# Kernel tuning notes

Hardware: AMD Instinct MI355X
Metric: run time of the kernel (lower is better)

The kernel has to match this reference:

```python
import jax, jax.numpy as jnp
import numpy as np

B, S, D = 16, 4096, 1024
K = 65536  # number of keys == number of concepts (identity mapping)
EPS = 1e-12


def setup_inputs() -> dict:
    key = jax.random.key(0)
    k1, k2, k3, k4, k5, k6 = jax.random.split(key, 6)
    return {
        "hidden": jax.random.normal(k1, (B, S, D), dtype=jnp.float32),
        "concept_signal": jax.random.normal(k2, (B, 1, D), dtype=jnp.float32),
        "keys": jax.random.normal(k3, (K, D), dtype=jnp.float32),
        "values": jax.random.normal(k4, (K, 1, D), dtype=jnp.float32),
        "key_to_value": jnp.arange(K, dtype=jnp.int64),
        "W_layer": jax.random.normal(k5, (D, D), dtype=jnp.float32) * 0.02,
        "b_layer": jax.random.normal(k6, (D,), dtype=jnp.float32) * 0.02,
    }


def _l2norm(x, axis=-1):
    return x / jnp.maximum(jnp.linalg.norm(x, axis=axis, keepdims=True), EPS)


def reference(hidden, concept_signal, keys, values, key_to_value, W_layer, b_layer):
    # self.layer(hidden_state): Linear(D, D)
    layer_out = jnp.einsum("bsd,ed->bse", hidden, W_layer) + b_layer  # [B, S, D]

    # Tensor branch of forward: per-sample nearest-key search.
    # q: one query position per sample (P=1) -> [B, D]
    q = concept_signal[:, 0, :]
    cos = jnp.einsum("bd,kd->bk", _l2norm(q), _l2norm(keys))  # cosine similarity [B, K]
    dist = 1.0 - cos                                           # cosine distance
    chosen_key = jnp.argmin(dist, axis=1)                      # [B] nearest key per sample
    # s = 1 - smallest_dist; with threshold=-2.0 it always passes; with
    # max_tokens_per_concept=1, k = max(1, ceil(clamp(s,0,1)*1)) == 1 token.
    concept_idx = key_to_value[chosen_key]                     # [B]
    tokens = values[concept_idx, 0, :]                         # [B, D] (first of the k=1 tokens)
    tokens = _l2norm(tokens)                                   # F.normalize(..., p=2, dim=-1)
    # vstack one token onto each sample, then stack -> [B, S+1, D]
    return jnp.concatenate([layer_out, tokens[:, None, :]], axis=1)
```

## Files before the change

kernel.cpp:

```cpp
#include <hip/hip_runtime.h>

constexpr int BB = 16;
constexpr int SS = 4096;
constexpr int DD = 1024;
constexpr int KK = 65536;
constexpr int GM = BB * SS;
constexpr int GK = DD;

typedef __attribute__((ext_vector_type(8))) short bf16x8;
typedef __attribute__((ext_vector_type(4))) float f32x4;
typedef __attribute__((ext_vector_type(8))) unsigned short ushort8;

#define GLD_LDS16(g, l)                                                        \
  __builtin_amdgcn_global_load_lds(                                            \
      (const __attribute__((address_space(1))) void*)(g),                      \
      (__attribute__((address_space(3))) void*)(l), 16, 0, 0)

__device__ __forceinline__ unsigned short f2bf(float x) {
  unsigned u = __float_as_uint(x);
  u += 0x7fffu + ((u >> 16) & 1u);
  return (unsigned short)(u >> 16);
}

__global__ void cvt_bf16(const float* __restrict__ in,
                         unsigned short* __restrict__ out, int n8) {
  int stride = gridDim.x * blockDim.x;
  for (int i = blockIdx.x * blockDim.x + threadIdx.x; i < n8; i += stride) {
    const float4* p = (const float4*)in + (size_t)i * 2;
    float4 a = p[0], b = p[1];
    ushort8 r;
    r[0] = f2bf(a.x); r[1] = f2bf(a.y); r[2] = f2bf(a.z); r[3] = f2bf(a.w);
    r[4] = f2bf(b.x); r[5] = f2bf(b.y); r[6] = f2bf(b.z); r[7] = f2bf(b.w);
    *(ushort8*)(out + (size_t)i * 8) = r;
  }
}

__global__ __launch_bounds__(256) void qt_prep(const float* __restrict__ csig,
                                               float* __restrict__ qT) {
  int e = blockIdx.x * 256 + threadIdx.x;
  int b = e >> 10, d = e & 1023;
  qT[d * 16 + b] = csig[e];
}

__global__ __launch_bounds__(256) void gemm_bt(
    const unsigned short* __restrict__ A,
    const unsigned short* __restrict__ Bm,
    const float* __restrict__ bias,
    float* __restrict__ out) {
  __shared__ unsigned short sA[128 * 32];
  __shared__ unsigned short sB[128 * 32];

  int g = blockIdx.x;
  int t = ((g & 7) << 9) + (g >> 3);
  int mt = t >> 3, nt = t & 7;
  int m0 = mt << 7, n0 = nt << 7;

  int tid = threadIdx.x, lane = tid & 63, wv = tid >> 6;
  int wr = wv >> 1, wc = wv & 1;
  int fr = lane & 15, ko = (lane >> 4) << 3;

  f32x4 acc[4][4] = {};

  int srow[2], scol[2];
  for (int i = 0; i < 2; ++i) {
    int off = (wv << 11) + (i << 10) + (lane << 4);
    srow[i] = off >> 6;
    scol[i] = (off & 63) >> 1;
  }

  for (int kt = 0; kt < GK / 32; ++kt) {
    int k0 = kt << 5;
    for (int i = 0; i < 2; ++i) {
      unsigned short* ldsA = sA + (wv << 10) + (i << 9);
      unsigned short* ldsB = sB + (wv << 10) + (i << 9);
      GLD_LDS16(A + (size_t)(m0 + srow[i]) * GK + k0 + scol[i], ldsA);
      GLD_LDS16(Bm + (size_t)(n0 + srow[i]) * GK + k0 + scol[i], ldsB);
    }
    __syncthreads();

    bf16x8 af[4], bfr[4];
#pragma unroll
    for (int i = 0; i < 4; ++i) {
      af[i]  = *(const bf16x8*)&sA[((wr << 6) + (i << 4) + fr) * 32 + ko];
      bfr[i] = *(const bf16x8*)&sB[((wc << 6) + (i << 4) + fr) * 32 + ko];
    }
#pragma unroll
    for (int m = 0; m < 4; ++m)
#pragma unroll
      for (int n = 0; n < 4; ++n)
        acc[m][n] = __builtin_amdgcn_mfma_f32_16x16x32_bf16(af[m], bfr[n],
                                                            acc[m][n], 0, 0, 0);
    __syncthreads();
  }

  int r0 = (lane >> 4) << 2, c = lane & 15;
#pragma unroll
  for (int n = 0; n < 4; ++n) {
    int gcol = n0 + (wc << 6) + (n << 4) + c;
    float bv = bias[gcol];
#pragma unroll
    for (int m = 0; m < 4; ++m) {
      int gr = m0 + (wr << 6) + (m << 4) + r0;
#pragma unroll
      for (int j = 0; j < 4; ++j) {
        int grow = gr + j;
        size_t o = ((size_t)(grow + (grow >> 12)) << 10) + gcol;
        out[o] = acc[m][n][j] + bv;
      }
    }
  }
}

__global__ __launch_bounds__(256) void cos_scores(
    const float* __restrict__ keys,
    const float* __restrict__ qT,
    float* __restrict__ pscore,
    int* __restrict__ pidx) {
  constexpr int DT = 32;
  __shared__ float kt[DT][256];
  __shared__ float rs[4][16];
  __shared__ int   ri[4][16];

  int tid = threadIdx.x, lane = tid & 63, w = tid >> 6;
  int k0 = blockIdx.x * 256;

  float acc[16] = {0.f, 0.f, 0.f, 0.f, 0.f, 0.f, 0.f, 0.f,
                   0.f, 0.f, 0.f, 0.f, 0.f, 0.f, 0.f, 0.f};
  float nrm = 0.f;

  int srow = tid >> 3, scol = (tid & 7) << 2;
  const float* gsrc = keys + (size_t)(k0 + srow) * DD + scol;

  float4 stg[8];
#pragma unroll
  for (int i = 0; i < 8; ++i)
    stg[i] = *(const float4*)(gsrc + (size_t)i * 32 * DD);

  for (int t = 0; t < DD / DT; ++t) {
#pragma unroll
    for (int i = 0; i < 8; ++i) {
      int r = (i << 5) + srow;
#pragma unroll
      for (int j = 0; j < 4; ++j) {
        int dd = scol + j;
        kt[dd][r ^ (((dd >> 2) & 7) << 2)] = stg[i][j];
      }
    }
    __syncthreads();

    if (t + 1 < DD / DT) {
      int d0n = (t + 1) * DT;
#pragma unroll
      for (int i = 0; i < 8; ++i)
        stg[i] = *(const float4*)(gsrc + (size_t)i * 32 * DD + d0n);
    }

    const float* qrow = qT + t * DT * 16;
#pragma unroll
    for (int dd = 0; dd < DT; ++dd) {
      float kv = kt[dd][tid ^ (((dd >> 2) & 7) << 2)];
      float4 q0 = *(const float4*)(qrow + dd * 16 + 0);
      float4 q1 = *(const float4*)(qrow + dd * 16 + 4);
      float4 q2 = *(const float4*)(qrow + dd * 16 + 8);
      float4 q3 = *(const float4*)(qrow + dd * 16 + 12);
      acc[0] = fmaf(kv, q0.x, acc[0]);   acc[1] = fmaf(kv, q0.y, acc[1]);
      acc[2] = fmaf(kv, q0.z, acc[2]);   acc[3] = fmaf(kv, q0.w, acc[3]);
      acc[4] = fmaf(kv, q1.x, acc[4]);   acc[5] = fmaf(kv, q1.y, acc[5]);
      acc[6] = fmaf(kv, q1.z, acc[6]);   acc[7] = fmaf(kv, q1.w, acc[7]);
      acc[8] = fmaf(kv, q2.x, acc[8]);   acc[9] = fmaf(kv, q2.y, acc[9]);
      acc[10] = fmaf(kv, q2.z, acc[10]); acc[11] = fmaf(kv, q2.w, acc[11]);
      acc[12] = fmaf(kv, q3.x, acc[12]); acc[13] = fmaf(kv, q3.y, acc[13]);
      acc[14] = fmaf(kv, q3.z, acc[14]); acc[15] = fmaf(kv, q3.w, acc[15]);
      nrm = fmaf(kv, kv, nrm);
    }
    __syncthreads();
  }

  float inv = rsqrtf(fmaxf(nrm, 1e-24f));
#pragma unroll
  for (int b = 0; b < 16; ++b) {
    float s = acc[b] * inv;
    int i = k0 + tid;
#pragma unroll
    for (int off = 32; off; off >>= 1) {
      float s2 = __shfl_xor(s, off);
      int i2 = __shfl_xor(i, off);
      if (s2 > s || (s2 == s && i2 < i)) { s = s2; i = i2; }
    }
    if (lane == 0) { rs[w][b] = s; ri[w][b] = i; }
  }
  __syncthreads();
  if (tid < 16) {
    float bs = rs[0][tid]; int bi = ri[0][tid];
#pragma unroll
    for (int w2 = 1; w2 < 4; ++w2) {
      float s = rs[w2][tid]; int i = ri[w2][tid];
      if (s > bs || (s == bs && i < bi)) { bs = s; bi = i; }
    }
    pscore[(size_t)tid * gridDim.x + blockIdx.x] = bs;
    pidx[(size_t)tid * gridDim.x + blockIdx.x] = bi;
  }
}

__global__ __launch_bounds__(256) void select_write(
    const float* __restrict__ pscore, const int* __restrict__ pidx, int nb,
    const int* __restrict__ ktv, const float* __restrict__ values,
    float* __restrict__ out) {
  __shared__ float ss[4];
  __shared__ int si[4];
  __shared__ float snrm;
  __shared__ int swin;
  int b = blockIdx.x, tid = threadIdx.x, lane = tid & 63, wv = tid >> 6;

  float best = -1e30f;
  int bidx = 0x7fffffff;
  for (int t = tid; t < nb; t += 256) {
    float s = pscore[(size_t)b * nb + t];
    int i = pidx[(size_t)b * nb + t];
    if (s > best || (s == best && i < bidx)) { best = s; bidx = i; }
  }
#pragma unroll
  for (int off = 32; off; off >>= 1) {
    float s = __shfl_xor(best, off);
    int i = __shfl_xor(bidx, off);
    if (s > best || (s == best && i < bidx)) { best = s; bidx = i; }
  }
  if (lane == 0) { ss[wv] = best; si[wv] = bidx; }
  __syncthreads();
  if (tid == 0) {
    float bs = ss[0]; int bi = si[0];
    for (int w2 = 1; w2 < 4; ++w2)
      if (ss[w2] > bs || (ss[w2] == bs && si[w2] < bi)) { bs = ss[w2]; bi = si[w2]; }
    swin = ktv[bi];
  }
  __syncthreads();
  int idx = swin;

  float4 v = ((const float4*)(values + (size_t)idx * DD))[tid];
  float nrm = v.x * v.x + v.y * v.y + v.z * v.z + v.w * v.w;
#pragma unroll
  for (int off = 32; off; off >>= 1) nrm += __shfl_xor(nrm, off);
  if (lane == 0) ss[wv] = nrm;
  __syncthreads();
  if (tid == 0) snrm = rsqrtf(fmaxf(ss[0] + ss[1] + ss[2] + ss[3], 1e-24f));
  __syncthreads();
  float inv = snrm;

  float4 o;
  o.x = v.x * inv; o.y = v.y * inv; o.z = v.z * inv; o.w = v.w * inv;
  ((float4*)(out + (((size_t)b * (SS + 1) + SS) << 10)))[tid] = o;
}

extern "C" void kernel_launch(void* const* d_in, const int* in_sizes, int n_in,
                              void* d_out, int out_size, void* d_ws,
                              size_t ws_size, hipStream_t stream) {
  const float* hidden = (const float*)d_in[0];
  const float* csig   = (const float*)d_in[1];
  const float* keys   = (const float*)d_in[2];
  const float* values = (const float*)d_in[3];
  const int*   ktv    = (const int*)d_in[4];
  const float* W      = (const float*)d_in[5];
  const float* bias   = (const float*)d_in[6];
  float* out = (float*)d_out;

  char* ws = (char*)d_ws;
  unsigned short* hbf = (unsigned short*)ws;
  unsigned short* wbf = (unsigned short*)(ws + (size_t)GM * GK * 2);
  char* p = ws + (size_t)GM * GK * 2 + (size_t)DD * GK * 2;
  float* pscore = (float*)p;
  int* pidx = (int*)(p + 16 * 256 * sizeof(float));
  float* qT = (float*)(p + 2 * 16 * 256 * sizeof(float));

  cvt_bf16<<<4096, 256, 0, stream>>>(hidden, hbf, GM * GK / 8);
  cvt_bf16<<<512, 256, 0, stream>>>(W, wbf, DD * GK / 8);
  qt_prep<<<64, 256, 0, stream>>>(csig, qT);

  cos_scores<<<256, 256, 0, stream>>>(keys, qT, pscore, pidx);

  gemm_bt<<<(GM / 128) * (DD / 128), 256, 0, stream>>>(hbf, wbf, bias, out);

  select_write<<<BB, 256, 0, stream>>>(pscore, pidx, 256, ktv, values, out);
}
```

Before: 464.9 us.

## Replace GEMM with 256x256 pipelined 8-wave kernel and split cosine search over D

The bf16 GEMM moves from a 128x128 tile with 4 waves and full-barrier k-steps to a 256x256 tile with 8 waves. It uses a 64-wide k, double-buffered swizzled LDS staging, interleaved async global-to-LDS loads, and setprio/sched_barrier phase scheduling, aiming to raise MFMA utilisation and operand reuse. Separately, the cosine key scan is split into four D-chunks across 1024 blocks with q staged in LDS, followed by a combine kernel that does the argmax. This is meant to fill more CUs than the old 256-block launch, at the cost of extra partial-sum traffic and one more launch.

```diff
diff --git a/kernel.cpp b/kernel.cpp
--- a/kernel.cpp
+++ b/kernel.cpp
@@ -42,101 +42,186 @@
   qT[d * 16 + b] = csig[e];
 }
 
-__global__ __launch_bounds__(256) void gemm_bt(
+
+#define LDA8(AH, BUF) do {                                                     \
+  _Pragma("unroll") for (int ms = 0; ms < 4; ++ms) {                           \
+    int rowa = (wm << 7) + ((AH) << 6) + (ms << 4) + fr;                       \
+    _Pragma("unroll") for (int ks = 0; ks < 2; ++ks) {                         \
+      int ia = ((rowa << 6) + (ks << 5) + (kg << 3)) ^ sw;                     \
+      ar[ms * 2 + ks] = *(const bf16x8*)&lds[(BUF) + ia]; } }                  \
+} while (0)
+
+#define LDB4(NP, BUF) do {                                                     \
+  _Pragma("unroll") for (int nn = 0; nn < 2; ++nn) {                           \
+    int rowb = (wn << 6) + ((((NP) << 1) + nn) << 4) + fr;                     \
+    _Pragma("unroll") for (int ks = 0; ks < 2; ++ks) {                         \
+      int ib = ((rowb << 6) + (ks << 5) + (kg << 3)) ^ sw;                     \
+      br[(((NP) << 1) + nn) * 2 + ks] = *(const bf16x8*)&lds[(BUF) + ib]; } }  \
+} while (0)
+
+#define MFMAQ(AH, NP) do {                                                     \
+  _Pragma("unroll") for (int ms = 0; ms < 4; ++ms)                             \
+  _Pragma("unroll") for (int nn = 0; nn < 2; ++nn)                             \
+  _Pragma("unroll") for (int ks = 0; ks < 2; ++ks)                             \
+    acc[((AH) << 2) + ms][((NP) << 1) + nn] =                                  \
+      __builtin_amdgcn_mfma_f32_16x16x32_bf16(ar[ms * 2 + ks],                 \
+        br[(((NP) << 1) + nn) * 2 + ks],                                       \
+        acc[((AH) << 2) + ms][((NP) << 1) + nn], 0, 0, 0);                     \
+} while (0)
+
+#define STAGEQ(GB, LB, QJ)                                                     \
+  GLD_LDS16((GB) + (size_t)(((QJ) << 6) + srq) * GK + ssc,                     \
+            &lds[(LB) + ((((QJ) << 9) + (wv << 6)) << 3)])
+
+#define PH_MID do { __builtin_amdgcn_s_barrier();                              \
+  asm volatile("s_waitcnt lgkmcnt(0)" ::: "memory");                           \
+  __builtin_amdgcn_sched_barrier(0);                                           \
+  __builtin_amdgcn_s_setprio(1); } while (0)
+
+#define PH_END do { __builtin_amdgcn_s_setprio(0);                             \
+  __builtin_amdgcn_s_barrier(); } while (0)
+
+#define PH_END_V(N) do { __builtin_amdgcn_s_setprio(0);                        \
+  asm volatile("s_waitcnt vmcnt(" #N ")" ::: "memory");                        \
+  __builtin_amdgcn_sched_barrier(0);                                           \
+  __builtin_amdgcn_s_barrier(); } while (0)
+
+__global__ __launch_bounds__(512, 2) void gemm8(
     const unsigned short* __restrict__ A,
     const unsigned short* __restrict__ Bm,
     const float* __restrict__ bias,
     float* __restrict__ out) {
-  __shared__ unsigned short sA[128 * 32];
-  __shared__ unsigned short sB[128 * 32];
+  __shared__ unsigned short lds[65536];
 
   int g = blockIdx.x;
-  int t = ((g & 7) << 9) + (g >> 3);
-  int mt = t >> 3, nt = t & 7;
-  int m0 = mt << 7, n0 = nt << 7;
+  int t = ((g & 7) << 7) + (g >> 3);
+  int mt = t >> 2, nt = t & 3;
+  int m0 = mt << 8, n0 = nt << 8;
 
   int tid = threadIdx.x, lane = tid & 63, wv = tid >> 6;
-  int wr = wv >> 1, wc = wv & 1;
-  int fr = lane & 15, ko = (lane >> 4) << 3;
-
-  f32x4 acc[4][4] = {};
-
-  int srow[2], scol[2];
-  for (int i = 0; i < 2; ++i) {
-    int off = (wv << 11) + (i << 10) + (lane << 4);
-    srow[i] = off >> 6;
-    scol[i] = (off & 63) >> 1;
-  }
-
-  for (int kt = 0; kt < GK / 32; ++kt) {
-    int k0 = kt << 5;
-    for (int i = 0; i < 2; ++i) {
-      unsigned short* ldsA = sA + (wv << 10) + (i << 9);
-      unsigned short* ldsB = sB + (wv << 10) + (i << 9);
-      GLD_LDS16(A + (size_t)(m0 + srow[i]) * GK + k0 + scol[i], ldsA);
-      GLD_LDS16(Bm + (size_t)(n0 + srow[i]) * GK + k0 + scol[i], ldsB);
-    }
-    __syncthreads();
-
-    bf16x8 af[4], bfr[4];
-#pragma unroll
-    for (int i = 0; i < 4; ++i) {
-      af[i]  = *(const bf16x8*)&sA[((wr << 6) + (i << 4) + fr) * 32 + ko];
-      bfr[i] = *(const bf16x8*)&sB[((wc << 6) + (i << 4) + fr) * 32 + ko];
-    }
-#pragma unroll
-    for (int m = 0; m < 4; ++m)
-#pragma unroll
-      for (int n = 0; n < 4; ++n)
-        acc[m][n] = __builtin_amdgcn_mfma_f32_16x16x32_bf16(af[m], bfr[n],
-                                                            acc[m][n], 0, 0, 0);
-    __syncthreads();
-  }
-
-  int r0 = (lane >> 4) << 2, c = lane & 15;
-#pragma unroll
-  for (int n = 0; n < 4; ++n) {
-    int gcol = n0 + (wc << 6) + (n << 4) + c;
+  int wm = wv >> 2, wn = wv & 3;
+  int fr = lane & 15, kg = lane >> 4;
+  int sw = (fr & 7) << 3;
+
+  int srq = (wv << 3) + (lane >> 3);
+  int ssc = (((lane & 7) ^ ((lane >> 3) & 7)) << 3);
+
+  const unsigned short* Ag = A + (size_t)m0 * GK;
+  const unsigned short* Bg = Bm + (size_t)n0 * GK;
+
+  f32x4 acc[8][4] = {};
+  bf16x8 ar[8], br[8];
+
+  {
+    const unsigned short* b0 = Bg;
+    const unsigned short* a1 = Ag + 64;
+    const unsigned short* b1 = Bg + 64;
+    STAGEQ(Ag, 0, 0); STAGEQ(Ag, 0, 1); STAGEQ(Ag, 0, 2); STAGEQ(Ag, 0, 3);
+    STAGEQ(b0, 16384, 0); STAGEQ(b0, 16384, 1);
+    STAGEQ(b0, 16384, 2); STAGEQ(b0, 16384, 3);
+    STAGEQ(a1, 32768, 0); STAGEQ(a1, 32768, 2);
+    STAGEQ(b1, 49152, 0); STAGEQ(b1, 49152, 1);
+    STAGEQ(b1, 49152, 2); STAGEQ(b1, 49152, 3);
+    asm volatile("s_waitcnt vmcnt(6)" ::: "memory");
+    __builtin_amdgcn_sched_barrier(0);
+    __builtin_amdgcn_s_barrier();
+  }
+
+  for (int i = 0; i < 7; ++i) {
+    const unsigned short* a1 = Ag + (size_t)(2 * i + 1) * 64;
+    const unsigned short* a2 = Ag + (size_t)(2 * i + 2) * 64;
+    const unsigned short* b2 = Bg + (size_t)(2 * i + 2) * 64;
+    const unsigned short* a3 = Ag + (size_t)(2 * i + 3) * 64;
+    const unsigned short* b3 = Bg + (size_t)(2 * i + 3) * 64;
+    LDA8(0, 0); LDB4(0, 16384);
+    STAGEQ(a1, 32768, 1); STAGEQ(a1, 32768, 3);
+    PH_MID; MFMAQ(0, 0); PH_END;
+    LDB4(1, 16384);
+    STAGEQ(a2, 0, 0); STAGEQ(a2, 0, 2);
+    PH_MID; MFMAQ(0, 1); PH_END;
+    LDA8(1, 0);
+    STAGEQ(b2, 16384, 0); STAGEQ(b2, 16384, 1);
+    PH_MID; MFMAQ(1, 0); PH_END;
+    STAGEQ(b2, 16384, 2); STAGEQ(b2, 16384, 3);
+    PH_MID; MFMAQ(1, 1); PH_END_V(6);
+    LDA8(0, 32768); LDB4(0, 49152);
+    STAGEQ(a2, 0, 1); STAGEQ(a2, 0, 3);
+    PH_MID; MFMAQ(0, 0); PH_END;
+    LDB4(1, 49152);
+    STAGEQ(a3, 32768, 0); STAGEQ(a3, 32768, 2);
+    PH_MID; MFMAQ(0, 1); PH_END;
+    LDA8(1, 32768);
+    STAGEQ(b3, 49152, 0); STAGEQ(b3, 49152, 1);
+    PH_MID; MFMAQ(1, 0); PH_END;
+    STAGEQ(b3, 49152, 2); STAGEQ(b3, 49152, 3);
+    PH_MID; MFMAQ(1, 1); PH_END_V(6);
+  }
+
+  {
+    const unsigned short* a15 = Ag + (size_t)15 * 64;
+    LDA8(0, 0); LDB4(0, 16384);
+    STAGEQ(a15, 32768, 1); STAGEQ(a15, 32768, 3);
+    PH_MID; MFMAQ(0, 0); PH_END;
+    LDB4(1, 16384); PH_MID; MFMAQ(0, 1); PH_END;
+    LDA8(1, 0);     PH_MID; MFMAQ(1, 0); PH_END;
+    PH_MID; MFMAQ(1, 1); PH_END_V(0);
+    LDA8(0, 32768); LDB4(0, 49152); PH_MID; MFMAQ(0, 0); PH_END;
+    LDB4(1, 49152); PH_MID; MFMAQ(0, 1); PH_END;
+    LDA8(1, 32768); PH_MID; MFMAQ(1, 0); PH_END;
+    PH_MID; MFMAQ(1, 1);
+    __builtin_amdgcn_s_setprio(0);
+  }
+
+  int r0 = kg << 2, cc = fr;
+#pragma unroll
+  for (int ni = 0; ni < 4; ++ni) {
+    int gcol = n0 + (wn << 6) + (ni << 4) + cc;
     float bv = bias[gcol];
 #pragma unroll
-    for (int m = 0; m < 4; ++m) {
-      int gr = m0 + (wr << 6) + (m << 4) + r0;
+    for (int mi = 0; mi < 8; ++mi) {
+      int gr = m0 + (wm << 7) + (mi << 4) + r0;
 #pragma unroll
       for (int j = 0; j < 4; ++j) {
         int grow = gr + j;
         size_t o = ((size_t)(grow + (grow >> 12)) << 10) + gcol;
-        out[o] = acc[m][n][j] + bv;
+        out[o] = acc[mi][ni][j] + bv;
       }
     }
   }
 }
 
-__global__ __launch_bounds__(256) void cos_scores(
+__global__ __launch_bounds__(256) void cos_part4(
     const float* __restrict__ keys,
     const float* __restrict__ qT,
-    float* __restrict__ pscore,
-    int* __restrict__ pidx) {
-  constexpr int DT = 32;
-  __shared__ float kt[DT][256];
-  __shared__ float rs[4][16];
-  __shared__ int   ri[4][16];
-
-  int tid = threadIdx.x, lane = tid & 63, w = tid >> 6;
-  int k0 = blockIdx.x * 256;
+    float* __restrict__ pd,
+    float* __restrict__ pn) {
+  __shared__ float kt[32][256];
+  __shared__ float qs[256 * 16];
+
+  int tid = threadIdx.x;
+  int kgrp = blockIdx.x & 255, dc = blockIdx.x >> 8;
+  int k0 = kgrp << 8, d0 = dc << 8;
+
+  {
+    const float4* src = (const float4*)(qT + (size_t)d0 * 16);
+    float4* dst = (float4*)qs;
+#pragma unroll
+    for (int i = 0; i < 4; ++i) dst[tid + i * 256] = src[tid + i * 256];
+  }
 
   float acc[16] = {0.f, 0.f, 0.f, 0.f, 0.f, 0.f, 0.f, 0.f,
                    0.f, 0.f, 0.f, 0.f, 0.f, 0.f, 0.f, 0.f};
   float nrm = 0.f;
 
   int srow = tid >> 3, scol = (tid & 7) << 2;
-  const float* gsrc = keys + (size_t)(k0 + srow) * DD + scol;
+  const float* gsrc = keys + (size_t)(k0 + srow) * DD + d0 + scol;
 
   float4 stg[8];
 #pragma unroll
   for (int i = 0; i < 8; ++i)
     stg[i] = *(const float4*)(gsrc + (size_t)i * 32 * DD);
 
-  for (int t = 0; t < DD / DT; ++t) {
+  for (int t = 0; t < 8; ++t) {
 #pragma unroll
     for (int i = 0; i < 8; ++i) {
       int r = (i << 5) + srow;
@@ -148,26 +233,25 @@
     }
     __syncthreads();
 
-    if (t + 1 < DD / DT) {
-      int d0n = (t + 1) * DT;
+    if (t + 1 < 8) {
 #pragma unroll
       for (int i = 0; i < 8; ++i)
-        stg[i] = *(const float4*)(gsrc + (size_t)i * 32 * DD + d0n);
-    }
-
-    const float* qrow = qT + t * DT * 16;
-#pragma unroll
-    for (int dd = 0; dd < DT; ++dd) {
+        stg[i] = *(const float4*)(gsrc + (size_t)i * 32 * DD + (t + 1) * 32);
+    }
+
+    const float* qb = qs + (t << 5) * 16;
+#pragma unroll
+    for (int dd = 0; dd < 32; ++dd) {
       float kv = kt[dd][tid ^ (((dd >> 2) & 7) << 2)];
-      float4 q0 = *(const float4*)(qrow + dd * 16 + 0);
-      float4 q1 = *(const float4*)(qrow + dd * 16 + 4);
-      float4 q2 = *(const float4*)(qrow + dd * 16 + 8);
-      float4 q3 = *(const float4*)(qrow + dd * 16 + 12);
-      acc[0] = fmaf(kv, q0.x, acc[0]);   acc[1] = fmaf(kv, q0.y, acc[1]);
-      acc[2] = fmaf(kv, q0.z, acc[2]);   acc[3] = fmaf(kv, q0.w, acc[3]);
-      acc[4] = fmaf(kv, q1.x, acc[4]);   acc[5] = fmaf(kv, q1.y, acc[5]);
-      acc[6] = fmaf(kv, q1.z, acc[6]);   acc[7] = fmaf(kv, q1.w, acc[7]);
-      acc[8] = fmaf(kv, q2.x, acc[8]);   acc[9] = fmaf(kv, q2.y, acc[9]);
+      float4 q0 = *(const float4*)(qb + dd * 16 + 0);
+      float4 q1 = *(const float4*)(qb + dd * 16 + 4);
+      float4 q2 = *(const float4*)(qb + dd * 16 + 8);
+      float4 q3 = *(const float4*)(qb + dd * 16 + 12);
+      acc[0]  = fmaf(kv, q0.x, acc[0]);  acc[1]  = fmaf(kv, q0.y, acc[1]);
+      acc[2]  = fmaf(kv, q0.z, acc[2]);  acc[3]  = fmaf(kv, q0.w, acc[3]);
+      acc[4]  = fmaf(kv, q1.x, acc[4]);  acc[5]  = fmaf(kv, q1.y, acc[5]);
+      acc[6]  = fmaf(kv, q1.z, acc[6]);  acc[7]  = fmaf(kv, q1.w, acc[7]);
+      acc[8]  = fmaf(kv, q2.x, acc[8]);  acc[9]  = fmaf(kv, q2.y, acc[9]);
       acc[10] = fmaf(kv, q2.z, acc[10]); acc[11] = fmaf(kv, q2.w, acc[11]);
       acc[12] = fmaf(kv, q3.x, acc[12]); acc[13] = fmaf(kv, q3.y, acc[13]);
       acc[14] = fmaf(kv, q3.z, acc[14]); acc[15] = fmaf(kv, q3.w, acc[15]);
@@ -176,11 +260,43 @@
     __syncthreads();
   }
 
+  int k = k0 + tid;
+  float4* po = (float4*)(pd + ((size_t)dc * KK + k) * 16);
+  po[0] = make_float4(acc[0], acc[1], acc[2], acc[3]);
+  po[1] = make_float4(acc[4], acc[5], acc[6], acc[7]);
+  po[2] = make_float4(acc[8], acc[9], acc[10], acc[11]);
+  po[3] = make_float4(acc[12], acc[13], acc[14], acc[15]);
+  pn[(size_t)dc * KK + k] = nrm;
+}
+
+__global__ __launch_bounds__(256) void cos_combine(
+    const float* __restrict__ pd, const float* __restrict__ pn,
+    float* __restrict__ pscore, int* __restrict__ pidx) {
+  __shared__ float rs[4][16];
+  __shared__ int ri[4][16];
+  int tid = threadIdx.x, lane = tid & 63, w = tid >> 6;
+  int k = blockIdx.x * 256 + tid;
+
+  float d[16] = {0.f, 0.f, 0.f, 0.f, 0.f, 0.f, 0.f, 0.f,
+                 0.f, 0.f, 0.f, 0.f, 0.f, 0.f, 0.f, 0.f};
+  float nrm = 0.f;
+#pragma unroll
+  for (int dc = 0; dc < 4; ++dc) {
+    const float4* p = (const float4*)(pd + ((size_t)dc * KK + k) * 16);
+#pragma unroll
+    for (int i = 0; i < 4; ++i) {
+      float4 v = p[i];
+      d[i * 4 + 0] += v.x; d[i * 4 + 1] += v.y;
+      d[i * 4 + 2] += v.z; d[i * 4 + 3] += v.w;
+    }
+    nrm += pn[(size_t)dc * KK + k];
+  }
   float inv = rsqrtf(fmaxf(nrm, 1e-24f));
+
 #pragma unroll
   for (int b = 0; b < 16; ++b) {
-    float s = acc[b] * inv;
-    int i = k0 + tid;
+    float s = d[b] * inv;
+    int i = k;
 #pragma unroll
     for (int off = 32; off; off >>= 1) {
       float s2 = __shfl_xor(s, off);
@@ -264,20 +380,23 @@
   float* out = (float*)d_out;
 
   char* ws = (char*)d_ws;
-  unsigned short* hbf = (unsigned short*)ws;
-  unsigned short* wbf = (unsigned short*)(ws + (size_t)GM * GK * 2);
-  char* p = ws + (size_t)GM * GK * 2 + (size_t)DD * GK * 2;
-  float* pscore = (float*)p;
-  int* pidx = (int*)(p + 16 * 256 * sizeof(float));
-  float* qT = (float*)(p + 2 * 16 * 256 * sizeof(float));
+  size_t off = 0;
+  unsigned short* hbf = (unsigned short*)(ws + off); off += (size_t)GM * GK * 2;
+  unsigned short* wbf = (unsigned short*)(ws + off); off += (size_t)DD * GK * 2;
+  float* pd     = (float*)(ws + off); off += (size_t)4 * KK * 16 * 4;
+  float* pn     = (float*)(ws + off); off += (size_t)4 * KK * 4;
+  float* pscore = (float*)(ws + off); off += (size_t)16 * 256 * 4;
+  int*   pidx   = (int*)(ws + off);   off += (size_t)16 * 256 * 4;
+  float* qT     = (float*)(ws + off); off += (size_t)DD * 16 * 4;
 
   cvt_bf16<<<4096, 256, 0, stream>>>(hidden, hbf, GM * GK / 8);
   cvt_bf16<<<512, 256, 0, stream>>>(W, wbf, DD * GK / 8);
   qt_prep<<<64, 256, 0, stream>>>(csig, qT);
 
-  cos_scores<<<256, 256, 0, stream>>>(keys, qT, pscore, pidx);
-
-  gemm_bt<<<(GM / 128) * (DD / 128), 256, 0, stream>>>(hbf, wbf, bias, out);
+  cos_part4<<<1024, 256, 0, stream>>>(keys, qT, pd, pn);
+  cos_combine<<<256, 256, 0, stream>>>(pd, pn, pscore, pidx);
+
+  gemm8<<<1024, 512, 0, stream>>>(hbf, wbf, bias, out);
 
   select_write<<<BB, 256, 0, stream>>>(pscore, pidx, 256, ktv, values, out);
 }
```

Result: faster. 396.5 us (-14.7%).
